# Kernel tuning notes

Hardware: AMD Instinct MI355X
Metric: run time of the kernel (lower is better)

The kernel has to match this reference:

```python
import jax, jax.numpy as jnp
import numpy as np

B, H, W, C = 64, 56, 56, 256
WIN, SHIFT, HEADS = 7, 3, 8
HEAD_DIM = C // HEADS
N = WIN * WIN
EPS = 1e-5


def _rel_pos_index():
    # matches get_relative_position_index (tf.meshgrid 'xy' indexing)
    xx, yy = np.meshgrid(np.arange(WIN), np.arange(WIN))  # shapes (W,H)
    coords = np.stack([yy, xx], 0).reshape(2, -1)  # (2, N)
    rel = coords[:, :, None] - coords[:, None, :]  # (2, N, N)
    rel = rel.transpose(1, 2, 0)
    idx = (rel[:, :, 0] + WIN - 1) * (2 * WIN - 1) + (rel[:, :, 1] + WIN - 1)
    return jnp.asarray(idx, dtype=jnp.int32)  # (N, N)


def _attn_mask():
    # shifted-window attention mask, (nW, N, N) with 0 / -100
    img = np.zeros((H, W), dtype=np.float32)
    cnt = 0
    for hs in (slice(0, -WIN), slice(-WIN, -SHIFT), slice(-SHIFT, None)):
        for ws in (slice(0, -WIN), slice(-WIN, -SHIFT), slice(-SHIFT, None)):
            img[hs, ws] = cnt
            cnt += 1
    mw = img.reshape(H // WIN, WIN, W // WIN, WIN).transpose(0, 2, 1, 3).reshape(-1, N)
    am = mw[:, None, :] - mw[:, :, None]
    am = np.where(am != 0, -100.0, 0.0).astype(np.float32)
    return jnp.asarray(am)  # (nW, N, N)


def _layer_norm(x, g, b):
    mu = jnp.mean(x, -1, keepdims=True)
    var = jnp.mean(jnp.square(x - mu), -1, keepdims=True)
    return (x - mu) * jax.lax.rsqrt(var + EPS) * g + b


def setup_inputs() -> dict:
    key = jax.random.key(0)
    ks = jax.random.split(key, 6)
    s = lambda fan: 1.0 / np.sqrt(fan)
    return {
        'x': jax.random.normal(ks[0], (B, H * W, C), jnp.float32),
        'ln1_g': jnp.ones((C,), jnp.float32),
        'ln1_b': jnp.zeros((C,), jnp.float32),
        'qkv_w': jax.random.normal(ks[1], (C, 3 * C), jnp.float32) * s(C),
        'qkv_b': jnp.zeros((3 * C,), jnp.float32),
        'rpb_table': jax.random.normal(ks[2], ((2 * WIN - 1) ** 2, HEADS), jnp.float32) * 0.02,
        'proj_w': jax.random.normal(ks[3], (C, C), jnp.float32) * s(C),
        'proj_b': jnp.zeros((C,), jnp.float32),
        'ln2_g': jnp.ones((C,), jnp.float32),
        'ln2_b': jnp.zeros((C,), jnp.float32),
        'mlp_w1': jax.random.normal(ks[4], (C, 4 * C), jnp.float32) * s(C),
        'mlp_b1': jnp.zeros((4 * C,), jnp.float32),
        'mlp_w2': jax.random.normal(ks[5], (4 * C, C), jnp.float32) * s(4 * C),
        'mlp_b2': jnp.zeros((C,), jnp.float32),
    }


def _forward(x, ln1_g, ln1_b, qkv_w, qkv_b, rpb_table, proj_w, proj_b,
             ln2_g, ln2_b, mlp_w1, mlp_b1, mlp_w2, mlp_b2):
    rel_idx = _rel_pos_index()
    mask = _attn_mask()
    nW = (H // WIN) * (W // WIN)

    shortcut = x
    y = _layer_norm(x, ln1_g, ln1_b).reshape(B, H, W, C)
    y = jnp.roll(y, (-SHIFT, -SHIFT), axis=(1, 2))
    # window partition -> (B*nW, N, C)
    y = y.reshape(B, H // WIN, WIN, W // WIN, WIN, C)
    y = y.transpose(0, 1, 3, 2, 4, 5).reshape(B * nW, N, C)

    qkv = (y @ qkv_w + qkv_b).reshape(B * nW, N, 3, HEADS, HEAD_DIM)
    q, k, v = jnp.moveaxis(qkv, 2, 0)  # each (B*nW, N, heads, hd)
    q = q * (HEAD_DIM ** -0.5)
    attn = jnp.einsum('wqhd,wkhd->whqk', q, k)  # (B*nW, heads, N, N)
    bias = jnp.transpose(rpb_table[rel_idx], (2, 0, 1))  # (heads, N, N)
    attn = attn + bias[None]
    attn = attn.reshape(B, nW, HEADS, N, N) + mask[None, :, None]
    attn = jax.nn.softmax(attn.reshape(B * nW, HEADS, N, N), axis=-1)
    o = jnp.einsum('whqk,wkhd->wqhd', attn, v).reshape(B * nW, N, C)
    o = o @ proj_w + proj_b

    # window reverse + un-shift
    o = o.reshape(B, H // WIN, W // WIN, WIN, WIN, C)
    o = o.transpose(0, 1, 3, 2, 4, 5).reshape(B, H, W, C)
    o = jnp.roll(o, (SHIFT, SHIFT), axis=(1, 2)).reshape(B, H * W, C)

    x = shortcut + o
    h = _layer_norm(x, ln2_g, ln2_b)
    h = jax.nn.gelu(h @ mlp_w1 + mlp_b1, approximate=False) @ mlp_w2 + mlp_b2
    return x + h


def reference(x, ln1_g, ln1_b, qkv_w, qkv_b, rpb_table, proj_w, proj_b,
              ln2_g, ln2_b, mlp_w1, mlp_b1, mlp_w2, mlp_b2):
    return _forward(x, ln1_g, ln1_b, qkv_w, qkv_b, rpb_table, proj_w, proj_b,
                    ln2_g, ln2_b, mlp_w1, mlp_b1, mlp_w2, mlp_b2)
```

## Files before the change

### kernel.cpp

```cpp
#include <hip/hip_runtime.h>
#include <math.h>


typedef __attribute__((ext_vector_type(8))) short bf16x8;
typedef __attribute__((ext_vector_type(4))) float f32x4;

#define NTOK 200704
#define NN   49
#define NPARAM 4680
#define TBL_ELEMS (4 * 8 * 49 * 64)

__device__ __forceinline__ float bf2f(unsigned short u) {
    union { unsigned int i; float f; } v; v.i = ((unsigned)u) << 16; return v.f;
}
__device__ __forceinline__ unsigned short f2bf(float f) {
    union { float fv; unsigned int i; } v; v.fv = f;
    return (unsigned short)((v.i + 0x7fffu + ((v.i >> 16) & 1u)) >> 16);
}

__device__ __forceinline__ void gload_lds16(const unsigned short* g, unsigned short* l) {
    __builtin_amdgcn_global_load_lds(
        (const __attribute__((address_space(1))) unsigned int*)g,
        (__attribute__((address_space(3))) unsigned int*)l, 16, 0, 0);
}

__device__ __forceinline__ float gelu_erf(float v) {
    float av = fabsf(v);
    float x = av * 0.70710678118654752f;
    float t = __builtin_amdgcn_rcpf(fmaf(x, 0.3275911f, 1.0f));
    float p = fmaf(1.061405429f, t, -1.453152027f);
    p = fmaf(p, t, 1.421413741f);
    p = fmaf(p, t, -0.284496736f);
    p = fmaf(p, t, 0.254829592f);
    p = p * t;
    float ex = __builtin_amdgcn_exp2f(x * x * -1.4426950408889634f);
    float E = fmaf(-p, ex, 1.0f);
    return fmaf(0.5f * av, E, 0.5f * v);
}

__global__ void detect_kernel(const unsigned short* __restrict__ xu, int* flag) {
    int ln = threadIdx.x;
    int sane = 0;
    #pragma unroll
    for (int t = 0; t < 16; t++) {
        unsigned u = xu[(ln * 16 + t) * 2];
        unsigned e = (u >> 7) & 0xFF;
        sane += (e >= 0x60 && e <= 0x90) ? 1 : 0;
    }
    #pragma unroll
    for (int off = 32; off; off >>= 1) sane += __shfl_xor(sane, off);
    if (ln == 0) *flag = (sane < 614) ? 1 : 0;
}

__device__ __forceinline__ float ld_any(const void* p, int j, int f) {
    return f ? ((const float*)p)[j] : bf2f(((const unsigned short*)p)[j]);
}

__global__ void convert_params_kernel(
    const void* ln1_g, const void* ln1_b, const void* qkv_b, const void* proj_b,
    const void* ln2_g, const void* ln2_b, const void* b1, const void* b2,
    const void* rpb, const int* __restrict__ flag, float* __restrict__ dst) {
    int i = blockIdx.x * 256 + threadIdx.x;
    if (i >= NPARAM) return;
    int f = *flag;
    const void* src; int j;
    if      (i < 256)  { src = ln1_g;  j = i; }
    else if (i < 512)  { src = ln1_b;  j = i - 256; }
    else if (i < 1280) { src = qkv_b;  j = i - 512; }
    else if (i < 1536) { src = proj_b; j = i - 1280; }
    else if (i < 1792) { src = ln2_g;  j = i - 1536; }
    else if (i < 2048) { src = ln2_b;  j = i - 1792; }
    else if (i < 3072) { src = b1;     j = i - 2048; }
    else if (i < 3328) { src = b2;     j = i - 3072; }
    else               { src = rpb;    j = i - 3328; }
    dst[i] = ld_any(src, j, f);
}

__global__ void build_tbl_kernel(const float* __restrict__ rpbF,
                                 float* __restrict__ tbl) {
    int idx = blockIdx.x * 256 + threadIdx.x;
    if (idx >= TBL_ELEMS) return;
    int k = idx & 63;
    int q = (idx >> 6) % 49;
    int h = ((idx >> 6) / 49) & 7;
    int pat = idx / (64 * 49 * 8);
    float v;
    if (k >= 49) {
        v = -1e30f;
    } else {
        int ir = q / 7, ic = q - ir * 7, jr = k / 7, jc = k - jr * 7;
        v = rpbF[((ir - jr + 6) * 13 + (ic - jc + 6)) * 8 + h];
        int rb = pat >> 1, cb = pat & 1;
        int ci = (rb ? (ir < 4 ? 3 : 6) : 0) + (cb ? (ic < 4 ? 1 : 2) : 0);
        int cj = (rb ? (jr < 4 ? 3 : 6) : 0) + (cb ? (jc < 4 ? 1 : 2) : 0);
        if (ci != cj) v -= 100.f;
    }
    tbl[idx] = v;
}

__global__ void transpose_any(const void* __restrict__ in,
                              unsigned short* __restrict__ out, int K, int N,
                              const int* __restrict__ flag) {
    int f = *flag;
    int idx = blockIdx.x * 256 + threadIdx.x;
    if (idx < K * N) {
        int k = idx / N, n = idx - k * N;
        out[n * K + k] = f2bf(ld_any(in, idx, f));
    }
}

__global__ void relayout_w1(const void* __restrict__ in,
                            unsigned short* __restrict__ out,
                            const int* __restrict__ flag) {
    int f = *flag;
    int idx = blockIdx.x * 256 + threadIdx.x;
    if (idx < 256 * 1024) {
        int k = idx >> 10, h = idx & 1023;
        int c = h >> 5, r = h & 31;
        int ks = k ^ ((r & 7) << 3);
        out[c * 8192 + r * 256 + ks] = f2bf(ld_any(in, idx, f));
    }
}

__global__ void relayout_w2(const void* __restrict__ in,
                            unsigned short* __restrict__ out,
                            const int* __restrict__ flag) {
    int f = *flag;
    int idx = blockIdx.x * 256 + threadIdx.x;
    if (idx < 1024 * 256) {
        int k = idx >> 8, n = idx & 255;
        int c = k >> 5, kk = k & 31;
        out[c * 8192 + n * 32 + kk] = f2bf(ld_any(in, idx, f));
    }
}

__global__ __launch_bounds__(256) void ln1_window_kernel(
    const void* __restrict__ x, const float* __restrict__ paramsF,
    unsigned short* __restrict__ y, const int* __restrict__ flag) {
    int f = *flag;
    int wv = threadIdx.x >> 6, ln = threadIdx.x & 63;
    int tok = blockIdx.x * 4 + wv;
    float v0, v1, v2, v3;
    if (f) {
        float4 pv = *(const float4*)((const float*)x + (size_t)tok * 256 + ln * 4);
        v0 = pv.x; v1 = pv.y; v2 = pv.z; v3 = pv.w;
    } else {
        ushort4 pv = *(const ushort4*)((const unsigned short*)x + (size_t)tok * 256 + ln * 4);
        v0 = bf2f(pv.x); v1 = bf2f(pv.y); v2 = bf2f(pv.z); v3 = bf2f(pv.w);
    }
    float s = v0 + v1 + v2 + v3;
    float sq = v0 * v0 + v1 * v1 + v2 * v2 + v3 * v3;
    #pragma unroll
    for (int off = 32; off; off >>= 1) { s += __shfl_xor(s, off); sq += __shfl_xor(sq, off); }
    float mu = s * (1.f / 256.f);
    float rs = rsqrtf(fmaxf(sq * (1.f / 256.f) - mu * mu, 0.f) + 1e-5f);
    float4 gv = *(const float4*)(paramsF + ln * 4);
    float4 bv = *(const float4*)(paramsF + 256 + ln * 4);
    int bb = tok / 3136, hw = tok - bb * 3136;
    int h = hw / 56, w = hw - h * 56;
    int hp = h - 3; hp += (hp < 0) ? 56 : 0;
    int wp = w - 3; wp += (wp < 0) ? 56 : 0;
    int win = (hp / 7) * 8 + (wp / 7);
    int n = (hp % 7) * 7 + (wp % 7);
    size_t drow = ((size_t)bb * 64 + win) * NN + n;
    ushort4 o;
    o.x = f2bf((v0 - mu) * rs * gv.x + bv.x);
    o.y = f2bf((v1 - mu) * rs * gv.y + bv.y);
    o.z = f2bf((v2 - mu) * rs * gv.z + bv.z);
    o.w = f2bf((v3 - mu) * rs * gv.w + bv.w);
    *(ushort4*)(y + drow * 256 + ln * 4) = o;
}

__device__ __forceinline__ void gemm_core_k256(
    const unsigned short* __restrict__ A, const unsigned short* __restrict__ Bt,
    int rowBase, int colBase, unsigned short* As, unsigned short* Bs, f32x4 acc[2][4]) {
    const int tid = threadIdx.x;
    const int wv = tid >> 6, ln = tid & 63;
    const int m16 = ln & 15, q4 = ln >> 4;
    const int ar = tid >> 1, ah = (tid & 1) * 32;
    const int br = tid >> 2, bp = (tid & 3) * 16;
    for (int kb = 0; kb < 256; kb += 64) {
        const unsigned short* ag = A + (size_t)(rowBase + ar) * 256 + kb + ah;
        unsigned short* asd = As + ar * 72 + ah;
        #pragma unroll
        for (int i = 0; i < 4; i++)
            *(bf16x8*)(asd + i * 8) = *(const bf16x8*)(ag + i * 8);
        const unsigned short* bg = Bt + (size_t)(colBase + br) * 256 + kb + bp;
        unsigned short* bsd = Bs + br * 72 + bp;
        #pragma unroll
        for (int i = 0; i < 2; i++)
            *(bf16x8*)(bsd + i * 8) = *(const bf16x8*)(bg + i * 8);
        __syncthreads();
        #pragma unroll
        for (int ks = 0; ks < 64; ks += 32) {
            bf16x8 af[2], bfr[4];
            #pragma unroll
            for (int rt = 0; rt < 2; rt++)
                af[rt] = *(const bf16x8*)(As + (wv * 32 + rt * 16 + m16) * 72 + ks + q4 * 8);
            #pragma unroll
            for (int ct = 0; ct < 4; ct++)
                bfr[ct] = *(const bf16x8*)(Bs + (ct * 16 + m16) * 72 + ks + q4 * 8);
            #pragma unroll
            for (int rt = 0; rt < 2; rt++)
                #pragma unroll
                for (int ct = 0; ct < 4; ct++)
                    acc[rt][ct] = __builtin_amdgcn_mfma_f32_16x16x32_bf16(
                        af[rt], bfr[ct], acc[rt][ct], 0, 0, 0);
        }
        __syncthreads();
    }
}

__global__ __launch_bounds__(256) void gemm_qkv_kernel(
    const unsigned short* __restrict__ A, const unsigned short* __restrict__ Bt,
    const float* __restrict__ bias,
    unsigned short* __restrict__ out) {
    __shared__ unsigned short As[128 * 72];
    __shared__ unsigned short Bs[64 * 72];
    const int ln = threadIdx.x & 63, wv = threadIdx.x >> 6;
    const int m16 = ln & 15, q4 = ln >> 4;
    const int rowBase = blockIdx.y * 128, colBase = blockIdx.x * 64;
    f32x4 acc[2][4];
    #pragma unroll
    for (int i = 0; i < 2; i++)
        #pragma unroll
        for (int j = 0; j < 4; j++)
            #pragma unroll
            for (int r = 0; r < 4; r++) acc[i][j][r] = 0.f;
    gemm_core_k256(A, Bt, rowBase, colBase, As, Bs, acc);
    #pragma unroll
    for (int rt = 0; rt < 2; rt++)
        #pragma unroll
        for (int ct = 0; ct < 4; ct++) {
            int col = colBase + ct * 16 + m16;
            float bs = bias[col];
            float scale = (col < 256) ? 0.17677669529663689f : 1.0f;
            #pragma unroll
            for (int r = 0; r < 4; r++) {
                int row = rowBase + wv * 32 + rt * 16 + q4 * 4 + r;
                out[(size_t)row * 768 + col] = f2bf((acc[rt][ct][r] + bs) * scale);
            }
        }
}

__global__ __launch_bounds__(256) void gemm_proj_kernel(
    const unsigned short* __restrict__ A, const unsigned short* __restrict__ Bt,
    const float* __restrict__ bias,
    const void* __restrict__ xin,
    unsigned short* __restrict__ x2, const int* __restrict__ flag) {
    __shared__ unsigned short As[128 * 72];
    __shared__ unsigned short Bs[64 * 72];
    const int f = *flag;
    const int ln = threadIdx.x & 63, wv = threadIdx.x >> 6;
    const int m16 = ln & 15, q4 = ln >> 4;
    const int rowBase = blockIdx.y * 128, colBase = blockIdx.x * 64;
    f32x4 acc[2][4];
    #pragma unroll
    for (int i = 0; i < 2; i++)
        #pragma unroll
        for (int j = 0; j < 4; j++)
            #pragma unroll
            for (int r = 0; r < 4; r++) acc[i][j][r] = 0.f;
    gemm_core_k256(A, Bt, rowBase, colBase, As, Bs, acc);
    #pragma unroll
    for (int rt = 0; rt < 2; rt++)
        #pragma unroll
        for (int r = 0; r < 4; r++) {
            int row = rowBase + wv * 32 + rt * 16 + q4 * 4 + r;
            int win = row / NN, n = row - win * NN;
            int bb = win >> 6, wl = win & 63;
            int i7 = n / 7, j7 = n - i7 * 7;
            int hp = (wl >> 3) * 7 + i7 + 3; if (hp >= 56) hp -= 56;
            int wp = (wl & 7) * 7 + j7 + 3;  if (wp >= 56) wp -= 56;
            size_t drow = ((size_t)bb * 3136 + hp * 56 + wp) * 256;
            #pragma unroll
            for (int ct = 0; ct < 4; ct++) {
                int col = colBase + ct * 16 + m16;
                float v = acc[rt][ct][r] + bias[col] + ld_any(xin, drow + col, f);
                x2[drow + col] = f2bf(v);
            }
        }
}

__global__ __launch_bounds__(256) void attn_mfma_kernel(
    const unsigned short* __restrict__ qkv,
    const float* __restrict__ tbl,
    unsigned short* __restrict__ o) {
    __shared__ __align__(16) unsigned short Vt[256 * 72];
    __shared__ __align__(16) unsigned short Ps[4][64 * 72];
    const int tid = threadIdx.x;
    const int wv = tid >> 6, ln = tid & 63;
    const int m16 = ln & 15, q4 = ln >> 4;
    const int win = blockIdx.x;
    const size_t wbase = (size_t)win * 49 * 768;

    #pragma unroll
    for (int i = 0; i < 8; i++) {
        int idx = i * 256 + tid;
        int ch = idx >> 6, tok = idx & 63;
        if (tok < 49) {
            bf16x8 v = *(const bf16x8*)(qkv + wbase + (size_t)tok * 768 + 512 + ch * 8);
            #pragma unroll
            for (int u = 0; u < 8; u++)
                Vt[(ch * 8 + u) * 72 + tok] = (unsigned short)v[u];
        }
    }
    #pragma unroll
    for (int u = 0; u < 23; u++) Vt[tid * 72 + 49 + u] = 0;

    const int wl = win & 63;
    const int pat = (((wl >> 3) == 7) ? 2 : 0) + (((wl & 7) == 7) ? 1 : 0);
    __syncthreads();

    unsigned short* Pw = &Ps[wv][0];
    for (int hh = 0; hh < 2; hh++) {
        const int h = wv * 2 + hh;
        bf16x8 kf[4], qf[4];
        #pragma unroll
        for (int t = 0; t < 4; t++) {
            size_t rrow = wbase + (size_t)(t * 16 + m16) * 768 + h * 32 + q4 * 8;
            qf[t] = *(const bf16x8*)(qkv + rrow);
            kf[t] = *(const bf16x8*)(qkv + rrow + 256);
        }
        f32x4 acc[4][4];
        #pragma unroll
        for (int kt = 0; kt < 4; kt++)
            #pragma unroll
            for (int qt = 0; qt < 4; qt++) {
                #pragma unroll
                for (int r = 0; r < 4; r++) acc[kt][qt][r] = 0.f;
                acc[kt][qt] = __builtin_amdgcn_mfma_f32_16x16x32_bf16(
                    kf[kt], qf[qt], acc[kt][qt], 0, 0, 0);
            }

        const float* tb = tbl + ((size_t)(pat * 8 + h) * 49) * 64;
        #pragma unroll
        for (int qt = 0; qt < 4; qt++) {
            int q = qt * 16 + m16;
            int qc = q < 49 ? q : 48;
            float s[4][4];
            float mx = -3e38f;
            #pragma unroll
            for (int kt = 0; kt < 4; kt++) {
                float4 tv = *(const float4*)(tb + qc * 64 + kt * 16 + q4 * 4);
                s[kt][0] = acc[kt][qt][0] + tv.x;
                s[kt][1] = acc[kt][qt][1] + tv.y;
                s[kt][2] = acc[kt][qt][2] + tv.z;
                s[kt][3] = acc[kt][qt][3] + tv.w;
                #pragma unroll
                for (int r = 0; r < 4; r++) mx = fmaxf(mx, s[kt][r]);
            }
            mx = fmaxf(mx, __shfl_xor(mx, 16));
            mx = fmaxf(mx, __shfl_xor(mx, 32));
            float sum = 0.f;
            #pragma unroll
            for (int kt = 0; kt < 4; kt++)
                #pragma unroll
                for (int r = 0; r < 4; r++) {
                    float e = __expf(s[kt][r] - mx);
                    s[kt][r] = e; sum += e;
                }
            sum += __shfl_xor(sum, 16);
            sum += __shfl_xor(sum, 32);
            float inv = 1.f / sum;
            #pragma unroll
            for (int kt = 0; kt < 4; kt++) {
                ushort4 p4;
                p4.x = f2bf(s[kt][0] * inv);
                p4.y = f2bf(s[kt][1] * inv);
                p4.z = f2bf(s[kt][2] * inv);
                p4.w = f2bf(s[kt][3] * inv);
                *(ushort4*)(Pw + q * 72 + kt * 16 + q4 * 4) = p4;
            }
        }

        f32x4 po[4][2];
        #pragma unroll
        for (int mt = 0; mt < 4; mt++)
            #pragma unroll
            for (int nt = 0; nt < 2; nt++)
                #pragma unroll
                for (int r = 0; r < 4; r++) po[mt][nt][r] = 0.f;
        #pragma unroll
        for (int kstep = 0; kstep < 2; kstep++) {
            bf16x8 pa[4], vb[2];
            #pragma unroll
            for (int mt = 0; mt < 4; mt++)
                pa[mt] = *(const bf16x8*)(Pw + (mt * 16 + m16) * 72 + kstep * 32 + q4 * 8);
            #pragma unroll
            for (int nt = 0; nt < 2; nt++)
                vb[nt] = *(const bf16x8*)(Vt + (h * 32 + nt * 16 + m16) * 72 + kstep * 32 + q4 * 8);
            #pragma unroll
            for (int mt = 0; mt < 4; mt++)
                #pragma unroll
                for (int nt = 0; nt < 2; nt++)
                    po[mt][nt] = __builtin_amdgcn_mfma_f32_16x16x32_bf16(
                        pa[mt], vb[nt], po[mt][nt], 0, 0, 0);
        }

        #pragma unroll
        for (int mt = 0; mt < 4; mt++)
            #pragma unroll
            for (int r = 0; r < 4; r++) {
                int q = mt * 16 + q4 * 4 + r;
                if (q < 49) {
                    size_t orow = ((size_t)win * 49 + q) * 256 + h * 32;
                    o[orow + m16]      = f2bf(po[mt][0][r]);
                    o[orow + 16 + m16] = f2bf(po[mt][1][r]);
                }
            }
    }
}

__global__ __launch_bounds__(256, 3) void mlp_fused_v4(
    const unsigned short* __restrict__ x2,
    const float* __restrict__ g2F, const float* __restrict__ b2lnF,
    const unsigned short* __restrict__ w1s,
    const float* __restrict__ b1F,
    const unsigned short* __restrict__ w2s,
    const float* __restrict__ b2F,
    void* __restrict__ out, const int* __restrict__ flag) {
    __shared__ __align__(16) unsigned short Bs1[2][32 * 256];
    const int f = *flag;
    const int tid = threadIdx.x;
    const int wv = tid >> 6, ln = tid & 63;
    const int m16 = ln & 15, q4 = ln >> 4;
    const int tok0 = blockIdx.x * 64;
    const int tok = tok0 + wv * 16 + m16;

    {
        const unsigned short* s1 = w1s + tid * 8;
        #pragma unroll
        for (int j = 0; j < 4; j++)
            gload_lds16(s1 + j * 2048, &Bs1[0][tid * 8 + j * 2048]);
    }

    bf16x8 areg[8];
    {
        const unsigned short* xr = x2 + (size_t)tok * 256 + q4 * 8;
        #pragma unroll
        for (int ks = 0; ks < 8; ks++) areg[ks] = *(const bf16x8*)(xr + ks * 32);
        float s = 0.f, sq = 0.f;
        #pragma unroll
        for (int ks = 0; ks < 8; ks++)
            #pragma unroll
            for (int u = 0; u < 8; u++) {
                float v = bf2f((unsigned short)areg[ks][u]);
                s += v; sq += v * v;
            }
        s += __shfl_xor(s, 16); s += __shfl_xor(s, 32);
        sq += __shfl_xor(sq, 16); sq += __shfl_xor(sq, 32);
        float mu = s * (1.f / 256.f);
        float rs = rsqrtf(fmaxf(sq * (1.f / 256.f) - mu * mu, 0.f) + 1e-5f);
        #pragma unroll
        for (int ks = 0; ks < 8; ks++)
            #pragma unroll
            for (int u = 0; u < 8; u++) {
                int kidx = ks * 32 + q4 * 8 + u;
                float v = (bf2f((unsigned short)areg[ks][u]) - mu) * rs * g2F[kidx] + b2lnF[kidx];
                areg[ks][u] = (short)f2bf(v);
            }
    }

    f32x4 acc2[16];
    #pragma unroll
    for (int i = 0; i < 16; i++)
        #pragma unroll
        for (int r = 0; r < 4; r++) acc2[i][r] = 0.f;

    const int l1 = m16 + (((2 * q4) & 3) << 4);
    const int l2 = m16 + (((2 * q4 + 1) & 3) << 4);
    const bool hi = q4 >= 2;

    #pragma unroll 1
    for (int c = 0; c < 32; ++c) {
        const int cur = c & 1;
        asm volatile("s_waitcnt vmcnt(0)" ::: "memory");
        __builtin_amdgcn_s_barrier();
        __builtin_amdgcn_sched_barrier(0);

        if (c + 1 < 32) {
            const unsigned short* s1 = w1s + (size_t)(c + 1) * 8192 + tid * 8;
            unsigned short* d1 = &Bs1[cur ^ 1][tid * 8];
            #pragma unroll
            for (int j = 0; j < 4; j++)
                gload_lds16(s1 + j * 2048, d1 + j * 2048);
        }
        __builtin_amdgcn_sched_barrier(0);

        f32x4 acc1[2];
        #pragma unroll
        for (int ct = 0; ct < 2; ct++)
            #pragma unroll
            for (int r = 0; r < 4; r++) acc1[ct][r] = 0.f;
        const unsigned short* b1base = &Bs1[cur][0];
        #pragma unroll
        for (int ks = 0; ks < 8; ks++) {
            int kidx = (ks * 32 + q4 * 8) ^ ((m16 & 7) << 3);
            #pragma unroll
            for (int ct = 0; ct < 2; ct++) {
                bf16x8 wfr = *(const bf16x8*)(b1base + (ct * 16 + m16) * 256 + kidx);
                acc1[ct] = __builtin_amdgcn_mfma_f32_16x16x32_bf16(wfr, areg[ks], acc1[ct], 0, 0, 0);
            }
        }

        union { ushort4 s; unsigned int u[2]; } pk[2];
        #pragma unroll
        for (int ct = 0; ct < 2; ct++) {
            float4 bb = *(const float4*)(b1F + c * 32 + ct * 16 + q4 * 4);
            pk[ct].s.x = f2bf(gelu_erf(acc1[ct][0] + bb.x));
            pk[ct].s.y = f2bf(gelu_erf(acc1[ct][1] + bb.y));
            pk[ct].s.z = f2bf(gelu_erf(acc1[ct][2] + bb.z));
            pk[ct].s.w = f2bf(gelu_erf(acc1[ct][3] + bb.w));
        }

        unsigned int r0x = __shfl(pk[0].u[0], l1), r0y = __shfl(pk[0].u[1], l1);
        unsigned int r0z = __shfl(pk[0].u[0], l2), r0w = __shfl(pk[0].u[1], l2);
        unsigned int r1x = __shfl(pk[1].u[0], l1), r1y = __shfl(pk[1].u[1], l1);
        unsigned int r1z = __shfl(pk[1].u[0], l2), r1w = __shfl(pk[1].u[1], l2);
        union { bf16x8 v; unsigned int u[4]; } bfrag;
        bfrag.u[0] = hi ? r1x : r0x;
        bfrag.u[1] = hi ? r1y : r0y;
        bfrag.u[2] = hi ? r1z : r0z;
        bfrag.u[3] = hi ? r1w : r0w;

        const unsigned short* w2g = w2s + (size_t)c * 8192 + m16 * 32 + q4 * 8;
        #pragma unroll
        for (int g = 0; g < 4; g++) {
            bf16x8 wf[4];
            #pragma unroll
            for (int j = 0; j < 4; j++)
                wf[j] = *(const bf16x8*)(w2g + (g * 4 + j) * 512);
            #pragma unroll
            for (int j = 0; j < 4; j++)
                acc2[g * 4 + j] = __builtin_amdgcn_mfma_f32_16x16x32_bf16(
                    wf[j], bfrag.v, acc2[g * 4 + j], 0, 0, 0);
        }
    }

    const size_t trow = (size_t)tok * 256;
    #pragma unroll
    for (int ct2 = 0; ct2 < 16; ct2++) {
        int col0 = ct2 * 16 + q4 * 4;
        float4 bb = *(const float4*)(b2F + col0);
        ushort4 rv = *(const ushort4*)(x2 + trow + col0);
        float v0 = acc2[ct2][0] + bb.x + bf2f(rv.x);
        float v1 = acc2[ct2][1] + bb.y + bf2f(rv.y);
        float v2 = acc2[ct2][2] + bb.z + bf2f(rv.z);
        float v3 = acc2[ct2][3] + bb.w + bf2f(rv.w);
        if (f) {
            float4 ov = {v0, v1, v2, v3};
            *(float4*)((float*)out + trow + col0) = ov;
        } else {
            ushort4 ov;
            ov.x = f2bf(v0); ov.y = f2bf(v1); ov.z = f2bf(v2); ov.w = f2bf(v3);
            *(ushort4*)((unsigned short*)out + trow + col0) = ov;
        }
    }
}

extern "C" void kernel_launch(void* const* d_in, const int* in_sizes, int n_in,
                              void* d_out, int out_size, void* d_ws, size_t ws_size,
                              hipStream_t stream) {
    const void* x      = d_in[0];
    const void* qkv_w  = d_in[3];
    const void* proj_w = d_in[6];
    const void* w1     = d_in[10];
    const void* w2     = d_in[12];

    char* ws = (char*)d_ws;
    size_t off = 0;
    unsigned short* y = (unsigned short*)(ws + off);
    off += (size_t)NTOK * 256 * 2;
    size_t qkv_off = off;
    unsigned short* qkv = (unsigned short*)(ws + off);
    off += (size_t)NTOK * 768 * 2;
    unsigned short* x2 = (unsigned short*)(ws + qkv_off);
    unsigned short* o = y;
    unsigned short* qkvWt = (unsigned short*)(ws + off); off += 768 * 256 * 2;
    unsigned short* projWt = (unsigned short*)(ws + off); off += 256 * 256 * 2;
    unsigned short* w1s = (unsigned short*)(ws + off); off += 1024 * 256 * 2;
    unsigned short* w2s = (unsigned short*)(ws + off); off += 256 * 1024 * 2;
    float* paramsF = (float*)(ws + off); off += NPARAM * 4;
    int* flag = (int*)(ws + off); off += 16;
    float* tbl = (float*)(ws + off); off += (size_t)TBL_ELEMS * 4;
    (void)ws_size; (void)in_sizes; (void)n_in; (void)out_size;

    detect_kernel<<<1, 64, 0, stream>>>((const unsigned short*)x, flag);
    convert_params_kernel<<<(NPARAM + 255) / 256, 256, 0, stream>>>(
        d_in[1], d_in[2], d_in[4], d_in[7], d_in[8], d_in[9], d_in[11], d_in[13],
        d_in[5], flag, paramsF);
    build_tbl_kernel<<<(TBL_ELEMS + 255) / 256, 256, 0, stream>>>(paramsF + 3328, tbl);
    transpose_any<<<(256 * 768 + 255) / 256, 256, 0, stream>>>(qkv_w, qkvWt, 256, 768, flag);
    transpose_any<<<(256 * 256 + 255) / 256, 256, 0, stream>>>(proj_w, projWt, 256, 256, flag);
    relayout_w1<<<(256 * 1024 + 255) / 256, 256, 0, stream>>>(w1, w1s, flag);
    relayout_w2<<<(1024 * 256 + 255) / 256, 256, 0, stream>>>(w2, w2s, flag);

    ln1_window_kernel<<<NTOK / 4, 256, 0, stream>>>(x, paramsF, y, flag);
    gemm_qkv_kernel<<<dim3(768 / 64, NTOK / 128), 256, 0, stream>>>(y, qkvWt, paramsF + 512, qkv);
    attn_mfma_kernel<<<4096, 256, 0, stream>>>(qkv, tbl, o);
    gemm_proj_kernel<<<dim3(256 / 64, NTOK / 128), 256, 0, stream>>>(
        o, projWt, paramsF + 1280, x, x2, flag);
    mlp_fused_v4<<<NTOK / 64, 256, 0, stream>>>(
        x2, paramsF + 1536, paramsF + 1792, w1s, paramsF + 2048, w2s, paramsF + 3072, d_out, flag);
}
```

Measured before the change: 1.499 ms.

## Stage W2 chunks in swizzled LDS and double MLP block to 128 tokens

The fused MLP kernel now uses 512-thread blocks covering 128 tokens. Each W1/W2 chunk is streamed into LDS once per block and shared by eight waves, where before W2 fragments were read straight from global memory by every wave. W2 is relaid with an XOR swizzle to avoid LDS bank conflicts, and s_setprio is raised around the MFMA sections. This cuts global/L2 traffic for W2 but doubles LDS use per block and changes occupancy to two 512-thread blocks per CU.

```diff
diff --git a/kernel.cpp b/kernel.cpp
--- a/kernel.cpp
+++ b/kernel.cpp
@@ -130,7 +130,8 @@
     if (idx < 1024 * 256) {
         int k = idx >> 8, n = idx & 255;
         int c = k >> 5, kk = k & 31;
-        out[c * 8192 + n * 32 + kk] = f2bf(ld_any(in, idx, f));
+        int slot = kk ^ ((n & 6) << 2);
+        out[c * 8192 + n * 32 + slot] = f2bf(ld_any(in, idx, f));
     }
 }
 
@@ -412,7 +413,7 @@
     }
 }
 
-__global__ __launch_bounds__(256, 3) void mlp_fused_v4(
+__global__ __launch_bounds__(512, 2) void mlp_fused_v5(
     const unsigned short* __restrict__ x2,
     const float* __restrict__ g2F, const float* __restrict__ b2lnF,
     const unsigned short* __restrict__ w1s,
@@ -421,18 +422,21 @@
     const float* __restrict__ b2F,
     void* __restrict__ out, const int* __restrict__ flag) {
     __shared__ __align__(16) unsigned short Bs1[2][32 * 256];
+    __shared__ __align__(16) unsigned short Bs2[2][256 * 32];
     const int f = *flag;
     const int tid = threadIdx.x;
     const int wv = tid >> 6, ln = tid & 63;
     const int m16 = ln & 15, q4 = ln >> 4;
-    const int tok0 = blockIdx.x * 64;
-    const int tok = tok0 + wv * 16 + m16;
+    const int tok = blockIdx.x * 128 + wv * 16 + m16;
 
     {
         const unsigned short* s1 = w1s + tid * 8;
-        #pragma unroll
-        for (int j = 0; j < 4; j++)
-            gload_lds16(s1 + j * 2048, &Bs1[0][tid * 8 + j * 2048]);
+        const unsigned short* s2 = w2s + tid * 8;
+        #pragma unroll
+        for (int j = 0; j < 2; j++) {
+            gload_lds16(s1 + j * 4096, &Bs1[0][tid * 8 + j * 4096]);
+            gload_lds16(s2 + j * 4096, &Bs2[0][tid * 8 + j * 4096]);
+        }
     }
 
     bf16x8 areg[8];
@@ -471,6 +475,7 @@
     const int l1 = m16 + (((2 * q4) & 3) << 4);
     const int l2 = m16 + (((2 * q4 + 1) & 3) << 4);
     const bool hi = q4 >= 2;
+    const int kswz2 = (m16 & 6) << 2;
 
     #pragma unroll 1
     for (int c = 0; c < 32; ++c) {
@@ -481,10 +486,14 @@
 
         if (c + 1 < 32) {
             const unsigned short* s1 = w1s + (size_t)(c + 1) * 8192 + tid * 8;
+            const unsigned short* s2 = w2s + (size_t)(c + 1) * 8192 + tid * 8;
             unsigned short* d1 = &Bs1[cur ^ 1][tid * 8];
-            #pragma unroll
-            for (int j = 0; j < 4; j++)
-                gload_lds16(s1 + j * 2048, d1 + j * 2048);
+            unsigned short* d2 = &Bs2[cur ^ 1][tid * 8];
+            #pragma unroll
+            for (int j = 0; j < 2; j++) {
+                gload_lds16(s1 + j * 4096, d1 + j * 4096);
+                gload_lds16(s2 + j * 4096, d2 + j * 4096);
+            }
         }
         __builtin_amdgcn_sched_barrier(0);
 
@@ -494,6 +503,7 @@
             #pragma unroll
             for (int r = 0; r < 4; r++) acc1[ct][r] = 0.f;
         const unsigned short* b1base = &Bs1[cur][0];
+        __builtin_amdgcn_s_setprio(1);
         #pragma unroll
         for (int ks = 0; ks < 8; ks++) {
             int kidx = (ks * 32 + q4 * 8) ^ ((m16 & 7) << 3);
@@ -503,6 +513,7 @@
                 acc1[ct] = __builtin_amdgcn_mfma_f32_16x16x32_bf16(wfr, areg[ks], acc1[ct], 0, 0, 0);
             }
         }
+        __builtin_amdgcn_s_setprio(0);
 
         union { ushort4 s; unsigned int u[2]; } pk[2];
         #pragma unroll
@@ -524,17 +535,19 @@
         bfrag.u[2] = hi ? r1z : r0z;
         bfrag.u[3] = hi ? r1w : r0w;
 
-        const unsigned short* w2g = w2s + (size_t)c * 8192 + m16 * 32 + q4 * 8;
+        const unsigned short* b2base = &Bs2[cur][0];
         #pragma unroll
         for (int g = 0; g < 4; g++) {
             bf16x8 wf[4];
             #pragma unroll
             for (int j = 0; j < 4; j++)
-                wf[j] = *(const bf16x8*)(w2g + (g * 4 + j) * 512);
+                wf[j] = *(const bf16x8*)(b2base + ((g * 4 + j) * 16 + m16) * 32 + ((q4 * 8) ^ kswz2));
+            __builtin_amdgcn_s_setprio(1);
             #pragma unroll
             for (int j = 0; j < 4; j++)
                 acc2[g * 4 + j] = __builtin_amdgcn_mfma_f32_16x16x32_bf16(
                     wf[j], bfrag.v, acc2[g * 4 + j], 0, 0, 0);
+            __builtin_amdgcn_s_setprio(0);
         }
     }
 
@@ -601,6 +614,6 @@
     attn_mfma_kernel<<<4096, 256, 0, stream>>>(qkv, tbl, o);
     gemm_proj_kernel<<<dim3(256 / 64, NTOK / 128), 256, 0, stream>>>(
         o, projWt, paramsF + 1280, x, x2, flag);
-    mlp_fused_v4<<<NTOK / 64, 256, 0, stream>>>(
+    mlp_fused_v5<<<NTOK / 128, 512, 0, stream>>>(
         x2, paramsF + 1536, paramsF + 1792, w1s, paramsF + 2048, w2s, paramsF + 3072, d_out, flag);
 }
```

Result: no change. 1.478 ms (-1.4%).
